# Performance work log

Measured on AMD Instinct MI355X. Metric: run time of the kernel, lower is better.

Reference implementation:

```python
import jax, jax.numpy as jnp
import numpy as np

NODES = 14      # input_size: nodes per graph
IN_F = 24       # seq_len: node feature dim
HID1 = 32
HID2 = 64       # hid_feats
HEADS = 2
OUT = 24        # output_size
B = 2048        # number of graphs
SLOPE = 0.2


def _make_edges():
    # fully connected (no self loops) within each 14-node graph
    pairs = np.array([(i, j) for i in range(NODES) for j in range(NODES) if i != j]).T  # [2,182]
    offs = (np.arange(B) * NODES)[:, None]
    src = (pairs[0][None, :] + offs).reshape(-1)
    dst = (pairs[1][None, :] + offs).reshape(-1)
    return np.stack([src, dst]).astype(np.int32)  # [2, 372736]


def setup_inputs() -> dict:
    key = jax.random.key(0)
    ks = jax.random.split(key, 16)
    N = B * NODES
    x = jax.random.normal(ks[0], (N, IN_F), dtype=jnp.float32)
    y = jax.random.normal(ks[1], (N, OUT), dtype=jnp.float32)
    edge_index = jnp.asarray(_make_edges())
    batch = jnp.repeat(jnp.arange(B, dtype=jnp.int32), NODES)
    s = 0.1
    params = dict(
        W1=jax.random.normal(ks[2], (IN_F, HEADS * HID1), dtype=jnp.float32) * s,
        a_src1=jax.random.normal(ks[3], (HEADS, HID1), dtype=jnp.float32) * s,
        a_dst1=jax.random.normal(ks[4], (HEADS, HID1), dtype=jnp.float32) * s,
        b1=jnp.zeros((HID1,), dtype=jnp.float32),
        W2=jax.random.normal(ks[5], (HID1, HEADS * HID2), dtype=jnp.float32) * s,
        a_src2=jax.random.normal(ks[6], (HEADS, HID2), dtype=jnp.float32) * s,
        a_dst2=jax.random.normal(ks[7], (HEADS, HID2), dtype=jnp.float32) * s,
        b2=jnp.zeros((HID2,), dtype=jnp.float32),
        Wf1=jax.random.normal(ks[8], (NODES, HID2, 8), dtype=jnp.float32) * s,
        bf1=jnp.zeros((NODES, 8), dtype=jnp.float32),
        Wf2=jax.random.normal(ks[9], (NODES, 8, OUT), dtype=jnp.float32) * s,
        bf2=jnp.zeros((NODES, OUT), dtype=jnp.float32),
    )
    return {"x": x, "y": y, "edge_index": edge_index, "batch": batch, **params}


def gat_conv(x, src, dst, W, a_src, a_dst, b):
    # PyG GATConv, concat=False (mean over heads), self-loops already in src/dst
    N = x.shape[0]
    H, F = a_src.shape
    xh = (x @ W).reshape(N, H, F)                       # [N,H,F]
    al_s = (xh * a_src).sum(-1)                         # [N,H]
    al_d = (xh * a_dst).sum(-1)                         # [N,H]
    alpha = jax.nn.leaky_relu(al_s[src] + al_d[dst], SLOPE)  # [E,H]
    amax = jax.ops.segment_max(alpha, dst, num_segments=N)
    ex = jnp.exp(alpha - amax[dst])
    den = jax.ops.segment_sum(ex, dst, num_segments=N)
    w = ex / den[dst]                                   # softmax per target node
    out = jax.ops.segment_sum(w[:, :, None] * xh[src], dst, num_segments=N)  # [N,H,F]
    return out.mean(axis=1) + b


def reference(x, y, edge_index, batch, W1, a_src1, a_dst1, b1, W2, a_src2, a_dst2, b2, Wf1, bf1, Wf2, bf2):
    N = x.shape[0]
    loops = jnp.arange(N, dtype=edge_index.dtype)
    src = jnp.concatenate([edge_index[0], loops])
    dst = jnp.concatenate([edge_index[1], loops])
    h = jax.nn.elu(gat_conv(x, src, dst, W1, a_src1, a_dst1, b1))   # [N,32]
    h = gat_conv(h, src, dst, W2, a_src2, a_dst2, b2)               # [N,64]
    # batch regroup: batch ids are contiguous per graph, so the Python
    # gather-loop in the original is exactly a reshape
    nb = N // NODES
    xg = h.reshape(nb, NODES, HID2).transpose(1, 0, 2)   # [14, B, 64]
    yg = y.reshape(nb, NODES, OUT)                       # [B, 14, out]
    # per-node-index MLP ensemble, batched over the 14 indices
    hh = jax.nn.relu(jnp.einsum('kbh,kho->kbo', xg, Wf1) + bf1[:, None, :])
    pred = jax.nn.sigmoid(jnp.einsum('kbo,kop->kbp', hh, Wf2) + bf2[:, None, :])  # [14,B,out]
    return pred, yg
```

## Files before the change

### kernel.cpp

```cpp
#include <hip/hip_runtime.h>

#define NODES 14
#define IN_F 24
#define HID1 32
#define HID2 64
#define OUT_F 24
#define SLOPE 0.2f

#define H1_S 36
#define H2_S 68

#define U_US1 0
#define U_UD1 48
#define U_US2 96
#define U_UD2 160

#define PHASE_FENCE() __builtin_amdgcn_sched_barrier(0)

__global__ __launch_bounds__(256) void compute_uvecs(
    const float* __restrict__ W1, const float* __restrict__ a_src1,
    const float* __restrict__ a_dst1,
    const float* __restrict__ W2, const float* __restrict__ a_src2,
    const float* __restrict__ a_dst2, float* __restrict__ u)
{
  const int tid = threadIdx.x;
  if (tid < 96) {
    const int sd = (tid >= 48), r = tid - sd * 48;
    const int h = (r >= IN_F), k = r - h * IN_F;
    const float* av = sd ? a_dst1 : a_src1;
    float s = 0.f;
#pragma unroll
    for (int f = 0; f < HID1; ++f)
      s += W1[k * 64 + h * HID1 + f] * av[h * HID1 + f];
    u[(sd ? U_UD1 : U_US1) + h * IN_F + k] = s;
  } else if (tid < 224) {
    const int j = tid - 96;
    const int sd = (j >= 64), r = j - sd * 64;
    const int h = (r >= HID1), k = r - h * HID1;
    const float* av = sd ? a_dst2 : a_src2;
    float s = 0.f;
#pragma unroll
    for (int f = 0; f < HID2; ++f)
      s += W2[k * 128 + h * HID2 + f] * av[h * HID2 + f];
    u[(sd ? U_UD2 : U_US2) + h * HID1 + k] = s;
  }
}

__global__ __launch_bounds__(128) void gnn_fused(
    const float* __restrict__ x, const float* __restrict__ y,
    const float* __restrict__ W1, const float* __restrict__ b1,
    const float* __restrict__ W2, const float* __restrict__ b2,
    const float* __restrict__ Wf1, const float* __restrict__ bf1,
    const float* __restrict__ Wf2, const float* __restrict__ bf2,
    const float* __restrict__ uvec,
    float* __restrict__ out, int ngraphs)
{
  const int g = blockIdx.x;
  const int tid = threadIdx.x;
  const int lane = tid & 63;
  const int wid = tid >> 6;

  __shared__ __align__(16) float h1s[NODES * H1_S];
  __shared__ __align__(16) float h2s[NODES * H2_S];
  __shared__ __align__(16) float wt[28 * 16];
  __shared__ __align__(16) float als[32], ald[32];
  __shared__ __align__(16) float hhs[112];

  const float* xg = x + (size_t)g * (NODES * IN_F);

  if (tid < (NODES * OUT_F) / 4) {
    const float4* y4 = (const float4*)(y + (size_t)g * (NODES * OUT_F));
    float4* o4 = (float4*)(out + (size_t)NODES * ngraphs * OUT_F
                               + (size_t)g * (NODES * OUT_F));
    o4[tid] = y4[tid];
  }

  float w1r[IN_F];
#pragma unroll
  for (int k = 0; k < IN_F; ++k) w1r[k] = W1[k * 64 + lane];
  float xcol[NODES];
#pragma unroll 2
  for (int n = 0; n < NODES; ++n) {
    float acc = 0.f;
#pragma unroll
    for (int k = 0; k < IN_F; ++k) acc += xg[n * IN_F + k] * w1r[k];
    xcol[n] = acc;
  }
  PHASE_FENCE();
  if (wid == 1) {
    if (lane < 56) {
      const int n = lane >> 2, h = (lane >> 1) & 1, sd = lane & 1;
      const float* uu = uvec + (sd ? U_UD1 : U_US1) + h * IN_F;
      float s = 0.f;
#pragma unroll
      for (int k4 = 0; k4 < 6; ++k4) {
        const float4 xv = *(const float4*)&xg[n * IN_F + k4 * 4];
        const float4 uv = *(const float4*)&uu[k4 * 4];
        s += xv.x * uv.x + xv.y * uv.y + xv.z * uv.z + xv.w * uv.w;
      }
      (sd ? ald : als)[h * 16 + n] = s;
    }
    if (lane < NODES * 2) {
      const int j = lane >> 1, h = lane & 1;
      const float ad = ald[h * 16 + j];
      const float4 A0 = *(const float4*)&als[h * 16 + 0];
      const float4 A1 = *(const float4*)&als[h * 16 + 4];
      const float4 A2 = *(const float4*)&als[h * 16 + 8];
      const float2 A3 = *(const float2*)&als[h * 16 + 12];
      float a[NODES] = {A0.x, A0.y, A0.z, A0.w, A1.x, A1.y, A1.z, A1.w,
                        A2.x, A2.y, A2.z, A2.w, A3.x, A3.y};
      float m = -1e30f;
#pragma unroll
      for (int i = 0; i < NODES; ++i) {
        float v = a[i] + ad;
        v = v > 0.f ? v : SLOPE * v;
        a[i] = v; m = fmaxf(m, v);
      }
      float den = 0.f;
#pragma unroll
      for (int i = 0; i < NODES; ++i) { a[i] = __expf(a[i] - m); den += a[i]; }
      const float r = 1.f / den;
      float* wr = &wt[lane * 16];
      *(float4*)&wr[0]  = make_float4(a[0]*r,  a[1]*r,  a[2]*r,  a[3]*r);
      *(float4*)&wr[4]  = make_float4(a[4]*r,  a[5]*r,  a[6]*r,  a[7]*r);
      *(float4*)&wr[8]  = make_float4(a[8]*r,  a[9]*r,  a[10]*r, a[11]*r);
      *(float2*)&wr[12] = make_float2(a[12]*r, a[13]*r);
    }
  }
  __syncthreads();
  PHASE_FENCE();

  {
    const int h = lane >> 5, f5 = lane & 31;
    const float bb = b1[f5];
#pragma unroll 2
    for (int tt = 0; tt < NODES / 2; ++tt) {
      const int n = wid * (NODES / 2) + tt;
      const float* wr = &wt[(n * 2 + h) * 16];
      const float4 w0 = *(const float4*)&wr[0];
      const float4 w1 = *(const float4*)&wr[4];
      const float4 w2 = *(const float4*)&wr[8];
      const float2 w3 = *(const float2*)&wr[12];
      float o = w0.x*xcol[0] + w0.y*xcol[1] + w0.z*xcol[2] + w0.w*xcol[3]
              + w1.x*xcol[4] + w1.y*xcol[5] + w1.z*xcol[6] + w1.w*xcol[7]
              + w2.x*xcol[8] + w2.y*xcol[9] + w2.z*xcol[10] + w2.w*xcol[11]
              + w3.x*xcol[12] + w3.y*xcol[13];
      const float oo = __shfl_xor(o, 32);
      if (h == 0) {
        const float v = 0.5f * (o + oo) + bb;
        h1s[n * H1_S + f5] = v > 0.f ? v : expm1f(v);
      }
    }
  }
  __syncthreads();
  PHASE_FENCE();

  float acc0[NODES], acc1[NODES];
  if (wid == 0) {
#pragma unroll
    for (int n = 0; n < NODES; ++n) { acc0[n] = 0.f; acc1[n] = 0.f; }
#pragma unroll
    for (int c = 0; c < 2; ++c) {
      float w2a[16], w2b[16];
#pragma unroll
      for (int j = 0; j < 16; ++j) {
        w2a[j] = W2[(c * 16 + j) * 128 + lane];
        w2b[j] = W2[(c * 16 + j) * 128 + 64 + lane];
      }
#pragma unroll 2
      for (int n = 0; n < NODES; ++n) {
        const float4 v0 = *(const float4*)&h1s[n * H1_S + c * 16 + 0];
        const float4 v1 = *(const float4*)&h1s[n * H1_S + c * 16 + 4];
        const float4 v2 = *(const float4*)&h1s[n * H1_S + c * 16 + 8];
        const float4 v3 = *(const float4*)&h1s[n * H1_S + c * 16 + 12];
        acc0[n] += v0.x*w2a[0] + v0.y*w2a[1] + v0.z*w2a[2] + v0.w*w2a[3]
                 + v1.x*w2a[4] + v1.y*w2a[5] + v1.z*w2a[6] + v1.w*w2a[7]
                 + v2.x*w2a[8] + v2.y*w2a[9] + v2.z*w2a[10] + v2.w*w2a[11]
                 + v3.x*w2a[12] + v3.y*w2a[13] + v3.z*w2a[14] + v3.w*w2a[15];
        acc1[n] += v0.x*w2b[0] + v0.y*w2b[1] + v0.z*w2b[2] + v0.w*w2b[3]
                 + v1.x*w2b[4] + v1.y*w2b[5] + v1.z*w2b[6] + v1.w*w2b[7]
                 + v2.x*w2b[8] + v2.y*w2b[9] + v2.z*w2b[10] + v2.w*w2b[11]
                 + v3.x*w2b[12] + v3.y*w2b[13] + v3.z*w2b[14] + v3.w*w2b[15];
      }
      PHASE_FENCE();
    }
  } else {
    if (lane < 56) {
      const int n = lane >> 2, h = (lane >> 1) & 1, sd = lane & 1;
      const float* uu = uvec + (sd ? U_UD2 : U_US2) + h * HID1;
      float s = 0.f;
#pragma unroll
      for (int k4 = 0; k4 < 8; ++k4) {
        const float4 hv = *(const float4*)&h1s[n * H1_S + k4 * 4];
        const float4 uv = *(const float4*)&uu[k4 * 4];
        s += hv.x * uv.x + hv.y * uv.y + hv.z * uv.z + hv.w * uv.w;
      }
      (sd ? ald : als)[h * 16 + n] = s;
    }
    if (lane < NODES * 2) {
      const int j = lane >> 1, h = lane & 1;
      const float ad = ald[h * 16 + j];
      const float4 A0 = *(const float4*)&als[h * 16 + 0];
      const float4 A1 = *(const float4*)&als[h * 16 + 4];
      const float4 A2 = *(const float4*)&als[h * 16 + 8];
      const float2 A3 = *(const float2*)&als[h * 16 + 12];
      float a[NODES] = {A0.x, A0.y, A0.z, A0.w, A1.x, A1.y, A1.z, A1.w,
                        A2.x, A2.y, A2.z, A2.w, A3.x, A3.y};
      float m = -1e30f;
#pragma unroll
      for (int i = 0; i < NODES; ++i) {
        float v = a[i] + ad;
        v = v > 0.f ? v : SLOPE * v;
        a[i] = v; m = fmaxf(m, v);
      }
      float den = 0.f;
#pragma unroll
      for (int i = 0; i < NODES; ++i) { a[i] = __expf(a[i] - m); den += a[i]; }
      const float r = 1.f / den;
      float* wr = &wt[lane * 16];
      *(float4*)&wr[0]  = make_float4(a[0]*r,  a[1]*r,  a[2]*r,  a[3]*r);
      *(float4*)&wr[4]  = make_float4(a[4]*r,  a[5]*r,  a[6]*r,  a[7]*r);
      *(float4*)&wr[8]  = make_float4(a[8]*r,  a[9]*r,  a[10]*r, a[11]*r);
      *(float2*)&wr[12] = make_float2(a[12]*r, a[13]*r);
    }
  }
  __syncthreads();
  PHASE_FENCE();

  if (wid == 0) {
    const float bb = b2[lane];
#pragma unroll 2
    for (int n = 0; n < NODES; ++n) {
      const float* wr0 = &wt[(n * 2 + 0) * 16];
      const float* wr1 = &wt[(n * 2 + 1) * 16];
      const float4 p0 = *(const float4*)&wr0[0];
      const float4 p1 = *(const float4*)&wr0[4];
      const float4 p2 = *(const float4*)&wr0[8];
      const float2 p3 = *(const float2*)&wr0[12];
      const float4 q0 = *(const float4*)&wr1[0];
      const float4 q1 = *(const float4*)&wr1[4];
      const float4 q2 = *(const float4*)&wr1[8];
      const float2 q3 = *(const float2*)&wr1[12];
      const float o0 = p0.x*acc0[0] + p0.y*acc0[1] + p0.z*acc0[2] + p0.w*acc0[3]
                     + p1.x*acc0[4] + p1.y*acc0[5] + p1.z*acc0[6] + p1.w*acc0[7]
                     + p2.x*acc0[8] + p2.y*acc0[9] + p2.z*acc0[10] + p2.w*acc0[11]
                     + p3.x*acc0[12] + p3.y*acc0[13];
      const float o1 = q0.x*acc1[0] + q0.y*acc1[1] + q0.z*acc1[2] + q0.w*acc1[3]
                     + q1.x*acc1[4] + q1.y*acc1[5] + q1.z*acc1[6] + q1.w*acc1[7]
                     + q2.x*acc1[8] + q2.y*acc1[9] + q2.z*acc1[10] + q2.w*acc1[11]
                     + q3.x*acc1[12] + q3.y*acc1[13];
      h2s[n * H2_S + lane] = 0.5f * (o0 + o1) + bb;
    }
  }
  __syncthreads();
  PHASE_FENCE();

  if (tid < NODES * 8) {
    const int k = tid >> 3, e = tid & 7;
    float acc = bf1[k * 8 + e];
#pragma unroll
    for (int f4 = 0; f4 < 16; ++f4) {
      const float4 hv = *(const float4*)&h2s[k * H2_S + f4 * 4];
      acc += hv.x * Wf1[(k * HID2 + f4 * 4 + 0) * 8 + e]
           + hv.y * Wf1[(k * HID2 + f4 * 4 + 1) * 8 + e]
           + hv.z * Wf1[(k * HID2 + f4 * 4 + 2) * 8 + e]
           + hv.w * Wf1[(k * HID2 + f4 * 4 + 3) * 8 + e];
    }
    hhs[tid] = fmaxf(acc, 0.f);
  }
  __syncthreads();
  PHASE_FENCE();

  for (int idx = tid; idx < NODES * OUT_F; idx += 128) {
    const int k = idx / OUT_F, o = idx - k * OUT_F;
    const float4 h0 = *(const float4*)&hhs[k * 8];
    const float4 h1 = *(const float4*)&hhs[k * 8 + 4];
    float acc = bf2[k * OUT_F + o]
              + h0.x * Wf2[(k * 8 + 0) * OUT_F + o]
              + h0.y * Wf2[(k * 8 + 1) * OUT_F + o]
              + h0.z * Wf2[(k * 8 + 2) * OUT_F + o]
              + h0.w * Wf2[(k * 8 + 3) * OUT_F + o]
              + h1.x * Wf2[(k * 8 + 4) * OUT_F + o]
              + h1.y * Wf2[(k * 8 + 5) * OUT_F + o]
              + h1.z * Wf2[(k * 8 + 6) * OUT_F + o]
              + h1.w * Wf2[(k * 8 + 7) * OUT_F + o];
    out[(size_t)k * ngraphs * OUT_F + (size_t)g * OUT_F + o] =
        1.f / (1.f + __expf(-acc));
  }
}

extern "C" void kernel_launch(void* const* d_in, const int* in_sizes, int n_in,
                              void* d_out, int out_size, void* d_ws, size_t ws_size,
                              hipStream_t stream) {
  const float* x      = (const float*)d_in[0];
  const float* y      = (const float*)d_in[1];
  const float* W1     = (const float*)d_in[4];
  const float* a_src1 = (const float*)d_in[5];
  const float* a_dst1 = (const float*)d_in[6];
  const float* b1     = (const float*)d_in[7];
  const float* W2     = (const float*)d_in[8];
  const float* a_src2 = (const float*)d_in[9];
  const float* a_dst2 = (const float*)d_in[10];
  const float* b2     = (const float*)d_in[11];
  const float* Wf1    = (const float*)d_in[12];
  const float* bf1    = (const float*)d_in[13];
  const float* Wf2    = (const float*)d_in[14];
  const float* bf2    = (const float*)d_in[15];
  float* out = (float*)d_out;
  float* u   = (float*)d_ws;

  const int nnodes  = in_sizes[0] / IN_F;
  const int ngraphs = nnodes / NODES;

  hipLaunchKernelGGL(compute_uvecs, dim3(1), dim3(256), 0, stream,
                     W1, a_src1, a_dst1, W2, a_src2, a_dst2, u);
  hipLaunchKernelGGL(gnn_fused, dim3(ngraphs), dim3(128), 0, stream,
                     x, y, W1, b1, W2, b2, Wf1, bf1, Wf2, bf2, u, out, ngraphs);
}
```

Before: 31.02 us.

## Map one graph per wavefront and drop block-wide barriers

Restructures the fused GAT kernel so each 64-lane wavefront processes a whole graph, with four graphs packed per 256-thread block and per-wave shared-memory slices. All __syncthreads calls are removed because each wave only touches its own LDS region, so the stages rely on in-wave execution order. The goal is to remove barrier stalls and the two-wave work split. In exchange each wave now serially does work that two waves shared, and correctness depends on LDS ordering within a wave, which normally holds since a wave's LDS operations complete in order.

```diff
diff --git a/kernel.cpp b/kernel.cpp
--- a/kernel.cpp
+++ b/kernel.cpp
@@ -7,14 +7,12 @@
 #define OUT_F 24
 #define SLOPE 0.2f
 
-#define H1_S 36
-#define H2_S 68
-
 #define U_US1 0
 #define U_UD1 48
 #define U_US2 96
 #define U_UD2 160
 
+#define GPB 4
 #define PHASE_FENCE() __builtin_amdgcn_sched_barrier(0)
 
 __global__ __launch_bounds__(256) void compute_uvecs(
@@ -46,7 +44,7 @@
   }
 }
 
-__global__ __launch_bounds__(128) void gnn_fused(
+__global__ __launch_bounds__(64 * GPB) void gnn_fused(
     const float* __restrict__ x, const float* __restrict__ y,
     const float* __restrict__ W1, const float* __restrict__ b1,
     const float* __restrict__ W2, const float* __restrict__ b2,
@@ -55,88 +53,89 @@
     const float* __restrict__ uvec,
     float* __restrict__ out, int ngraphs)
 {
-  const int g = blockIdx.x;
-  const int tid = threadIdx.x;
+  const int tid  = threadIdx.x;
   const int lane = tid & 63;
-  const int wid = tid >> 6;
-
-  __shared__ __align__(16) float h1s[NODES * H1_S];
-  __shared__ __align__(16) float h2s[NODES * H2_S];
-  __shared__ __align__(16) float wt[28 * 16];
-  __shared__ __align__(16) float als[32], ald[32];
-  __shared__ __align__(16) float hhs[112];
-
-  const float* xg = x + (size_t)g * (NODES * IN_F);
-
-  if (tid < (NODES * OUT_F) / 4) {
-    const float4* y4 = (const float4*)(y + (size_t)g * (NODES * OUT_F));
+  const int wv   = tid >> 6;
+  const int gu   = __builtin_amdgcn_readfirstlane(blockIdx.x * GPB + wv);
+  if (gu >= ngraphs) return;
+
+  __shared__ __align__(16) float h1s[GPB][NODES * 32];
+  __shared__ __align__(16) float h2s[GPB][NODES * 64];
+  __shared__ __align__(16) float wt[GPB][28 * 16];
+  __shared__ __align__(16) float als[GPB][32];
+  __shared__ __align__(16) float ald[GPB][32];
+  __shared__ __align__(16) float hhs[GPB][112];
+
+  const float* xg = x + (size_t)gu * (NODES * IN_F);
+
+  {
+    const float4* y4 = (const float4*)(y + (size_t)gu * (NODES * OUT_F));
     float4* o4 = (float4*)(out + (size_t)NODES * ngraphs * OUT_F
-                               + (size_t)g * (NODES * OUT_F));
-    o4[tid] = y4[tid];
-  }
-
-  float w1r[IN_F];
-#pragma unroll
-  for (int k = 0; k < IN_F; ++k) w1r[k] = W1[k * 64 + lane];
+                               + (size_t)gu * (NODES * OUT_F));
+    for (int i = lane; i < (NODES * OUT_F) / 4; i += 64) o4[i] = y4[i];
+  }
+
   float xcol[NODES];
+  {
+    float w1r[IN_F];
+#pragma unroll
+    for (int k = 0; k < IN_F; ++k) w1r[k] = W1[k * 64 + lane];
 #pragma unroll 2
-  for (int n = 0; n < NODES; ++n) {
-    float acc = 0.f;
-#pragma unroll
-    for (int k = 0; k < IN_F; ++k) acc += xg[n * IN_F + k] * w1r[k];
-    xcol[n] = acc;
-  }
-  PHASE_FENCE();
-  if (wid == 1) {
-    if (lane < 56) {
-      const int n = lane >> 2, h = (lane >> 1) & 1, sd = lane & 1;
-      const float* uu = uvec + (sd ? U_UD1 : U_US1) + h * IN_F;
-      float s = 0.f;
-#pragma unroll
-      for (int k4 = 0; k4 < 6; ++k4) {
-        const float4 xv = *(const float4*)&xg[n * IN_F + k4 * 4];
-        const float4 uv = *(const float4*)&uu[k4 * 4];
-        s += xv.x * uv.x + xv.y * uv.y + xv.z * uv.z + xv.w * uv.w;
-      }
-      (sd ? ald : als)[h * 16 + n] = s;
-    }
-    if (lane < NODES * 2) {
-      const int j = lane >> 1, h = lane & 1;
-      const float ad = ald[h * 16 + j];
-      const float4 A0 = *(const float4*)&als[h * 16 + 0];
-      const float4 A1 = *(const float4*)&als[h * 16 + 4];
-      const float4 A2 = *(const float4*)&als[h * 16 + 8];
-      const float2 A3 = *(const float2*)&als[h * 16 + 12];
-      float a[NODES] = {A0.x, A0.y, A0.z, A0.w, A1.x, A1.y, A1.z, A1.w,
-                        A2.x, A2.y, A2.z, A2.w, A3.x, A3.y};
-      float m = -1e30f;
-#pragma unroll
-      for (int i = 0; i < NODES; ++i) {
-        float v = a[i] + ad;
-        v = v > 0.f ? v : SLOPE * v;
-        a[i] = v; m = fmaxf(m, v);
-      }
-      float den = 0.f;
-#pragma unroll
-      for (int i = 0; i < NODES; ++i) { a[i] = __expf(a[i] - m); den += a[i]; }
-      const float r = 1.f / den;
-      float* wr = &wt[lane * 16];
-      *(float4*)&wr[0]  = make_float4(a[0]*r,  a[1]*r,  a[2]*r,  a[3]*r);
-      *(float4*)&wr[4]  = make_float4(a[4]*r,  a[5]*r,  a[6]*r,  a[7]*r);
-      *(float4*)&wr[8]  = make_float4(a[8]*r,  a[9]*r,  a[10]*r, a[11]*r);
-      *(float2*)&wr[12] = make_float2(a[12]*r, a[13]*r);
-    }
-  }
-  __syncthreads();
+    for (int n = 0; n < NODES; ++n) {
+      float acc = 0.f;
+#pragma unroll
+      for (int k = 0; k < IN_F; ++k) acc += xg[n * IN_F + k] * w1r[k];
+      xcol[n] = acc;
+    }
+  }
+  PHASE_FENCE();
+
+  if (lane < 56) {
+    const int n = lane >> 2, h = (lane >> 1) & 1, sd = lane & 1;
+    const float* uu = uvec + (sd ? U_UD1 : U_US1) + h * IN_F;
+    float s = 0.f;
+#pragma unroll
+    for (int k4 = 0; k4 < 6; ++k4) {
+      const float4 xv = *(const float4*)&xg[n * IN_F + k4 * 4];
+      const float4 uv = *(const float4*)&uu[k4 * 4];
+      s += xv.x * uv.x + xv.y * uv.y + xv.z * uv.z + xv.w * uv.w;
+    }
+    (sd ? ald : als)[wv][h * 16 + n] = s;
+  }
+  if (lane < NODES * 2) {
+    const int j = lane >> 1, h = lane & 1;
+    const float ad = ald[wv][h * 16 + j];
+    const float4 A0 = *(const float4*)&als[wv][h * 16 + 0];
+    const float4 A1 = *(const float4*)&als[wv][h * 16 + 4];
+    const float4 A2 = *(const float4*)&als[wv][h * 16 + 8];
+    const float2 A3 = *(const float2*)&als[wv][h * 16 + 12];
+    float a[NODES] = {A0.x, A0.y, A0.z, A0.w, A1.x, A1.y, A1.z, A1.w,
+                      A2.x, A2.y, A2.z, A2.w, A3.x, A3.y};
+    float m = -1e30f;
+#pragma unroll
+    for (int i = 0; i < NODES; ++i) {
+      float v = a[i] + ad;
+      v = v > 0.f ? v : SLOPE * v;
+      a[i] = v; m = fmaxf(m, v);
+    }
+    float den = 0.f;
+#pragma unroll
+    for (int i = 0; i < NODES; ++i) { a[i] = __expf(a[i] - m); den += a[i]; }
+    const float r = 1.f / den;
+    float* wr = &wt[wv][(j * 2 + h) * 16];
+    *(float4*)&wr[0]  = make_float4(a[0]*r,  a[1]*r,  a[2]*r,  a[3]*r);
+    *(float4*)&wr[4]  = make_float4(a[4]*r,  a[5]*r,  a[6]*r,  a[7]*r);
+    *(float4*)&wr[8]  = make_float4(a[8]*r,  a[9]*r,  a[10]*r, a[11]*r);
+    *(float2*)&wr[12] = make_float2(a[12]*r, a[13]*r);
+  }
   PHASE_FENCE();
 
   {
     const int h = lane >> 5, f5 = lane & 31;
     const float bb = b1[f5];
 #pragma unroll 2
-    for (int tt = 0; tt < NODES / 2; ++tt) {
-      const int n = wid * (NODES / 2) + tt;
-      const float* wr = &wt[(n * 2 + h) * 16];
+    for (int n = 0; n < NODES; ++n) {
+      const float* wr = &wt[wv][(n * 2 + h) * 16];
       const float4 w0 = *(const float4*)&wr[0];
       const float4 w1 = *(const float4*)&wr[4];
       const float4 w2 = *(const float4*)&wr[8];
@@ -148,91 +147,87 @@
       const float oo = __shfl_xor(o, 32);
       if (h == 0) {
         const float v = 0.5f * (o + oo) + bb;
-        h1s[n * H1_S + f5] = v > 0.f ? v : expm1f(v);
+        h1s[wv][n * 32 + f5] = v > 0.f ? v : expm1f(v);
       }
     }
   }
-  __syncthreads();
   PHASE_FENCE();
 
   float acc0[NODES], acc1[NODES];
-  if (wid == 0) {
-#pragma unroll
-    for (int n = 0; n < NODES; ++n) { acc0[n] = 0.f; acc1[n] = 0.f; }
-#pragma unroll
-    for (int c = 0; c < 2; ++c) {
-      float w2a[16], w2b[16];
-#pragma unroll
-      for (int j = 0; j < 16; ++j) {
-        w2a[j] = W2[(c * 16 + j) * 128 + lane];
-        w2b[j] = W2[(c * 16 + j) * 128 + 64 + lane];
-      }
+#pragma unroll
+  for (int n = 0; n < NODES; ++n) { acc0[n] = 0.f; acc1[n] = 0.f; }
+#pragma unroll
+  for (int c = 0; c < 2; ++c) {
+    float w2a[16], w2b[16];
+#pragma unroll
+    for (int j = 0; j < 16; ++j) {
+      w2a[j] = W2[(c * 16 + j) * 128 + lane];
+      w2b[j] = W2[(c * 16 + j) * 128 + 64 + lane];
+    }
 #pragma unroll 2
-      for (int n = 0; n < NODES; ++n) {
-        const float4 v0 = *(const float4*)&h1s[n * H1_S + c * 16 + 0];
-        const float4 v1 = *(const float4*)&h1s[n * H1_S + c * 16 + 4];
-        const float4 v2 = *(const float4*)&h1s[n * H1_S + c * 16 + 8];
-        const float4 v3 = *(const float4*)&h1s[n * H1_S + c * 16 + 12];
-        acc0[n] += v0.x*w2a[0] + v0.y*w2a[1] + v0.z*w2a[2] + v0.w*w2a[3]
-                 + v1.x*w2a[4] + v1.y*w2a[5] + v1.z*w2a[6] + v1.w*w2a[7]
-                 + v2.x*w2a[8] + v2.y*w2a[9] + v2.z*w2a[10] + v2.w*w2a[11]
-                 + v3.x*w2a[12] + v3.y*w2a[13] + v3.z*w2a[14] + v3.w*w2a[15];
-        acc1[n] += v0.x*w2b[0] + v0.y*w2b[1] + v0.z*w2b[2] + v0.w*w2b[3]
-                 + v1.x*w2b[4] + v1.y*w2b[5] + v1.z*w2b[6] + v1.w*w2b[7]
-                 + v2.x*w2b[8] + v2.y*w2b[9] + v2.z*w2b[10] + v2.w*w2b[11]
-                 + v3.x*w2b[12] + v3.y*w2b[13] + v3.z*w2b[14] + v3.w*w2b[15];
-      }
-      PHASE_FENCE();
-    }
-  } else {
-    if (lane < 56) {
-      const int n = lane >> 2, h = (lane >> 1) & 1, sd = lane & 1;
-      const float* uu = uvec + (sd ? U_UD2 : U_US2) + h * HID1;
-      float s = 0.f;
-#pragma unroll
-      for (int k4 = 0; k4 < 8; ++k4) {
-        const float4 hv = *(const float4*)&h1s[n * H1_S + k4 * 4];
-        const float4 uv = *(const float4*)&uu[k4 * 4];
-        s += hv.x * uv.x + hv.y * uv.y + hv.z * uv.z + hv.w * uv.w;
-      }
-      (sd ? ald : als)[h * 16 + n] = s;
-    }
-    if (lane < NODES * 2) {
-      const int j = lane >> 1, h = lane & 1;
-      const float ad = ald[h * 16 + j];
-      const float4 A0 = *(const float4*)&als[h * 16 + 0];
-      const float4 A1 = *(const float4*)&als[h * 16 + 4];
-      const float4 A2 = *(const float4*)&als[h * 16 + 8];
-      const float2 A3 = *(const float2*)&als[h * 16 + 12];
-      float a[NODES] = {A0.x, A0.y, A0.z, A0.w, A1.x, A1.y, A1.z, A1.w,
-                        A2.x, A2.y, A2.z, A2.w, A3.x, A3.y};
-      float m = -1e30f;
-#pragma unroll
-      for (int i = 0; i < NODES; ++i) {
-        float v = a[i] + ad;
-        v = v > 0.f ? v : SLOPE * v;
-        a[i] = v; m = fmaxf(m, v);
-      }
-      float den = 0.f;
-#pragma unroll
-      for (int i = 0; i < NODES; ++i) { a[i] = __expf(a[i] - m); den += a[i]; }
-      const float r = 1.f / den;
-      float* wr = &wt[lane * 16];
-      *(float4*)&wr[0]  = make_float4(a[0]*r,  a[1]*r,  a[2]*r,  a[3]*r);
-      *(float4*)&wr[4]  = make_float4(a[4]*r,  a[5]*r,  a[6]*r,  a[7]*r);
-      *(float4*)&wr[8]  = make_float4(a[8]*r,  a[9]*r,  a[10]*r, a[11]*r);
-      *(float2*)&wr[12] = make_float2(a[12]*r, a[13]*r);
-    }
-  }
-  __syncthreads();
-  PHASE_FENCE();
-
-  if (wid == 0) {
+    for (int n = 0; n < NODES; ++n) {
+      const float4 v0 = *(const float4*)&h1s[wv][n * 32 + c * 16 + 0];
+      const float4 v1 = *(const float4*)&h1s[wv][n * 32 + c * 16 + 4];
+      const float4 v2 = *(const float4*)&h1s[wv][n * 32 + c * 16 + 8];
+      const float4 v3 = *(const float4*)&h1s[wv][n * 32 + c * 16 + 12];
+      acc0[n] += v0.x*w2a[0] + v0.y*w2a[1] + v0.z*w2a[2] + v0.w*w2a[3]
+               + v1.x*w2a[4] + v1.y*w2a[5] + v1.z*w2a[6] + v1.w*w2a[7]
+               + v2.x*w2a[8] + v2.y*w2a[9] + v2.z*w2a[10] + v2.w*w2a[11]
+               + v3.x*w2a[12] + v3.y*w2a[13] + v3.z*w2a[14] + v3.w*w2a[15];
+      acc1[n] += v0.x*w2b[0] + v0.y*w2b[1] + v0.z*w2b[2] + v0.w*w2b[3]
+               + v1.x*w2b[4] + v1.y*w2b[5] + v1.z*w2b[6] + v1.w*w2b[7]
+               + v2.x*w2b[8] + v2.y*w2b[9] + v2.z*w2b[10] + v2.w*w2b[11]
+               + v3.x*w2b[12] + v3.y*w2b[13] + v3.z*w2b[14] + v3.w*w2b[15];
+    }
+    PHASE_FENCE();
+  }
+
+  if (lane < 56) {
+    const int n = lane >> 2, h = (lane >> 1) & 1, sd = lane & 1;
+    const float* uu = uvec + (sd ? U_UD2 : U_US2) + h * HID1;
+    float s = 0.f;
+#pragma unroll
+    for (int k4 = 0; k4 < 8; ++k4) {
+      const float4 hv = *(const float4*)&h1s[wv][n * 32 + k4 * 4];
+      const float4 uv = *(const float4*)&uu[k4 * 4];
+      s += hv.x * uv.x + hv.y * uv.y + hv.z * uv.z + hv.w * uv.w;
+    }
+    (sd ? ald : als)[wv][h * 16 + n] = s;
+  }
+  if (lane < NODES * 2) {
+    const int j = lane >> 1, h = lane & 1;
+    const float ad = ald[wv][h * 16 + j];
+    const float4 A0 = *(const float4*)&als[wv][h * 16 + 0];
+    const float4 A1 = *(const float4*)&als[wv][h * 16 + 4];
+    const float4 A2 = *(const float4*)&als[wv][h * 16 + 8];
+    const float2 A3 = *(const float2*)&als[wv][h * 16 + 12];
+    float a[NODES] = {A0.x, A0.y, A0.z, A0.w, A1.x, A1.y, A1.z, A1.w,
+                      A2.x, A2.y, A2.z, A2.w, A3.x, A3.y};
+    float m = -1e30f;
+#pragma unroll
+    for (int i = 0; i < NODES; ++i) {
+      float v = a[i] + ad;
+      v = v > 0.f ? v : SLOPE * v;
+      a[i] = v; m = fmaxf(m, v);
+    }
+    float den = 0.f;
+#pragma unroll
+    for (int i = 0; i < NODES; ++i) { a[i] = __expf(a[i] - m); den += a[i]; }
+    const float r = 1.f / den;
+    float* wr = &wt[wv][(j * 2 + h) * 16];
+    *(float4*)&wr[0]  = make_float4(a[0]*r,  a[1]*r,  a[2]*r,  a[3]*r);
+    *(float4*)&wr[4]  = make_float4(a[4]*r,  a[5]*r,  a[6]*r,  a[7]*r);
+    *(float4*)&wr[8]  = make_float4(a[8]*r,  a[9]*r,  a[10]*r, a[11]*r);
+    *(float2*)&wr[12] = make_float2(a[12]*r, a[13]*r);
+  }
+  PHASE_FENCE();
+
+  {
     const float bb = b2[lane];
 #pragma unroll 2
     for (int n = 0; n < NODES; ++n) {
-      const float* wr0 = &wt[(n * 2 + 0) * 16];
-      const float* wr1 = &wt[(n * 2 + 1) * 16];
+      const float* wr0 = &wt[wv][(n * 2 + 0) * 16];
+      const float* wr1 = &wt[wv][(n * 2 + 1) * 16];
       const float4 p0 = *(const float4*)&wr0[0];
       const float4 p1 = *(const float4*)&wr0[4];
       const float4 p2 = *(const float4*)&wr0[8];
@@ -249,32 +244,30 @@
                      + q1.x*acc1[4] + q1.y*acc1[5] + q1.z*acc1[6] + q1.w*acc1[7]
                      + q2.x*acc1[8] + q2.y*acc1[9] + q2.z*acc1[10] + q2.w*acc1[11]
                      + q3.x*acc1[12] + q3.y*acc1[13];
-      h2s[n * H2_S + lane] = 0.5f * (o0 + o1) + bb;
-    }
-  }
-  __syncthreads();
-  PHASE_FENCE();
-
-  if (tid < NODES * 8) {
-    const int k = tid >> 3, e = tid & 7;
+      h2s[wv][n * 64 + lane] = 0.5f * (o0 + o1) + bb;
+    }
+  }
+  PHASE_FENCE();
+
+  for (int idx = lane; idx < NODES * 8; idx += 64) {
+    const int k = idx >> 3, e = idx & 7;
     float acc = bf1[k * 8 + e];
 #pragma unroll
     for (int f4 = 0; f4 < 16; ++f4) {
-      const float4 hv = *(const float4*)&h2s[k * H2_S + f4 * 4];
+      const float4 hv = *(const float4*)&h2s[wv][k * 64 + f4 * 4];
       acc += hv.x * Wf1[(k * HID2 + f4 * 4 + 0) * 8 + e]
            + hv.y * Wf1[(k * HID2 + f4 * 4 + 1) * 8 + e]
            + hv.z * Wf1[(k * HID2 + f4 * 4 + 2) * 8 + e]
            + hv.w * Wf1[(k * HID2 + f4 * 4 + 3) * 8 + e];
     }
-    hhs[tid] = fmaxf(acc, 0.f);
-  }
-  __syncthreads();
-  PHASE_FENCE();
-
-  for (int idx = tid; idx < NODES * OUT_F; idx += 128) {
+    hhs[wv][idx] = fmaxf(acc, 0.f);
+  }
+  PHASE_FENCE();
+
+  for (int idx = lane; idx < NODES * OUT_F; idx += 64) {
     const int k = idx / OUT_F, o = idx - k * OUT_F;
-    const float4 h0 = *(const float4*)&hhs[k * 8];
-    const float4 h1 = *(const float4*)&hhs[k * 8 + 4];
+    const float4 h0 = *(const float4*)&hhs[wv][k * 8];
+    const float4 h1 = *(const float4*)&hhs[wv][k * 8 + 4];
     float acc = bf2[k * OUT_F + o]
               + h0.x * Wf2[(k * 8 + 0) * OUT_F + o]
               + h0.y * Wf2[(k * 8 + 1) * OUT_F + o]
@@ -284,7 +277,7 @@
               + h1.y * Wf2[(k * 8 + 5) * OUT_F + o]
               + h1.z * Wf2[(k * 8 + 6) * OUT_F + o]
               + h1.w * Wf2[(k * 8 + 7) * OUT_F + o];
-    out[(size_t)k * ngraphs * OUT_F + (size_t)g * OUT_F + o] =
+    out[(size_t)k * ngraphs * OUT_F + (size_t)gu * OUT_F + o] =
         1.f / (1.f + __expf(-acc));
   }
 }
@@ -311,9 +304,10 @@
 
   const int nnodes  = in_sizes[0] / IN_F;
   const int ngraphs = nnodes / NODES;
+  const int nblocks = (ngraphs + GPB - 1) / GPB;
 
   hipLaunchKernelGGL(compute_uvecs, dim3(1), dim3(256), 0, stream,
                      W1, a_src1, a_dst1, W2, a_src2, a_dst2, u);
-  hipLaunchKernelGGL(gnn_fused, dim3(ngraphs), dim3(128), 0, stream,
+  hipLaunchKernelGGL(gnn_fused, dim3(nblocks), dim3(64 * GPB), 0, stream,
                      x, y, W1, b1, W2, b2, Wf1, bf1, Wf2, bf2, u, out, ngraphs);
 }
```

Measured after the change: 33.25 us. 7.2% more time.
